# Performance work log

Hardware: AMD Instinct MI355X
Metric: run time of the kernel (lower is better)

The kernel has to match this reference:

```python
import jax, jax.numpy as jnp
import numpy as np

B, C, H, W = 4, 256, 64, 64
C8 = C // 8


def setup_inputs() -> dict:
    key = jax.random.key(0)
    ks = jax.random.split(key, 8)
    x = jax.random.normal(ks[0], (B, C, H, W), dtype=jnp.float32)
    valid = jax.random.uniform(ks[1], (B, 1, H, W), dtype=jnp.float32)
    # 1x1 conv weights (kernel_size=1 -> plain channel matmul) + biases
    Wq = jax.random.normal(ks[2], (C8, C), dtype=jnp.float32) * 0.05
    bq = jnp.zeros((C8,), dtype=jnp.float32)
    Wk = jax.random.normal(ks[3], (C8, C), dtype=jnp.float32) * 0.05
    bk = jnp.zeros((C8,), dtype=jnp.float32)
    Wv = jax.random.normal(ks[4], (C, C), dtype=jnp.float32) * 0.05
    bv = jnp.zeros((C,), dtype=jnp.float32)
    gamma = jnp.asarray(0.5, dtype=jnp.float32)  # nonzero so attention path matters
    return {"x": x, "valid": valid, "Wq": Wq, "bq": bq, "Wk": Wk, "bk": bk,
            "Wv": Wv, "bv": bv, "gamma": gamma}


def reference(x, valid, Wq, bq, Wk, bk, Wv, bv, gamma):
    b, c, h, w = x.shape
    n = h * w
    xf = x.reshape(b, c, n)                                   # [B,C,N]
    # valid is already at (H,W): nearest interpolate to same size is identity
    v = valid.reshape(b, 1, n)                                # [B,1,N]
    q = jnp.einsum('oc,bcn->bno', Wq, xf) + bq                # [B,N,C//8]
    k = jnp.einsum('oc,bcn->bon', Wk, xf) + bk[None, :, None] # [B,C//8,N]
    energy = jnp.einsum('bno,bom->bnm', q, k)                 # [B,N,N]
    attn = jax.nn.softmax(energy, axis=-1)
    va = attn * v                                             # mask columns
    scale = 1.0 / jnp.sum(va, axis=2, keepdims=True)          # per-row renorm
    sa = va * scale                                           # [B,N,N]
    pv = jnp.einsum('oc,bcn->bon', Wv, xf) + bv[None, :, None]  # [B,C,N]
    out = jnp.einsum('bon,bmn->bom', pv, sa)                  # bmm(V, A^T)
    out = out.reshape(b, c, h, w)
    return gamma * out + x, sa
```

## Files before the change

### kernel.cpp

```cpp
#include <hip/hip_runtime.h>

typedef unsigned short u16;
typedef unsigned int u32;
typedef __attribute__((ext_vector_type(8))) short short8;
typedef __attribute__((ext_vector_type(4))) float f32x4;
typedef __attribute__((ext_vector_type(2))) unsigned int u32x2;
typedef __attribute__((ext_vector_type(4))) unsigned int u32x4;

#define BB 4
#define CC 256
#define NT 4096
#define L2E 1.4426950408889634f

__device__ __forceinline__ float b2f(u16 v) {
    union { u32 u; float f; } c; c.u = ((u32)v) << 16; return c.f;
}
__device__ __forceinline__ u16 f2b(float f) {
    union { float f; u32 u; } c; c.f = f;
    u32 u = c.u;
    return (u16)((u + 0x7fffu + ((u >> 16) & 1u)) >> 16);
}

__global__ __launch_bounds__(256) void kprep(
    const float* __restrict__ Wq, const float* __restrict__ Wk,
    const float* __restrict__ Wv, const float* __restrict__ bq,
    const float* __restrict__ bk_, const float* __restrict__ bv,
    u16* __restrict__ wh, u16* __restrict__ wl, float* __restrict__ biasAll)
{
    const int bkx = blockIdx.x;
    const int t = threadIdx.x;
    #pragma unroll
    for (int j = 0; j < 4; ++j) {
        const int idx4 = t + 256 * j;
        const int row  = bkx * 16 + (idx4 >> 6);
        const int col4 = (idx4 & 63) * 4;
        const float* src = row < 32 ? Wq + row * 256
                         : row < 64 ? Wk + (row - 32) * 256
                         :            Wv + (row - 64) * 256;
        f32x4 v = *(const f32x4*)(src + col4);
        u16 h[4], l[4];
        #pragma unroll
        for (int i = 0; i < 4; ++i) {
            h[i] = f2b(v[i]);
            l[i] = f2b(v[i] - b2f(h[i]));
        }
        u32x2 ph, pl;
        ph[0] = (u32)h[0] | ((u32)h[1] << 16); ph[1] = (u32)h[2] | ((u32)h[3] << 16);
        pl[0] = (u32)l[0] | ((u32)l[1] << 16); pl[1] = (u32)l[2] | ((u32)l[3] << 16);
        *(u32x2*)(wh + row * 256 + col4) = ph;
        *(u32x2*)(wl + row * 256 + col4) = pl;
    }
    if (t < 16) {
        const int row = bkx * 16 + t;
        biasAll[row] = row < 32 ? bq[row] : row < 64 ? bk_[row - 32] : bv[row - 64];
    }
}

__global__ __launch_bounds__(256, 1) void kproj(
    const float* __restrict__ x,
    const u16* __restrict__ wh, const u16* __restrict__ wl,
    const float* __restrict__ biasAll,
    u16* __restrict__ qh, u16* __restrict__ ql,
    u16* __restrict__ kh, u16* __restrict__ kl,
    u16* __restrict__ pvw)
{
    __shared__ __align__(16) float lX[256][68];
    __shared__ float lbias[320];
    const int b = blockIdx.y, n0 = blockIdx.x * 64;
    const int t = threadIdx.x;
    const int lane = t & 63, wv = t >> 6;
    const int quad = lane >> 4, l16 = lane & 15;

    {
        const int kX = t >> 3, nn8 = (t & 7) * 8;
        const float* xrow = x + ((size_t)(b * CC + kX)) * NT + n0 + nn8;
        #pragma unroll
        for (int k0 = 0; k0 < 256; k0 += 32) {
            f32x4 xa = *(const f32x4*)(xrow + (size_t)k0 * NT);
            f32x4 xb = *(const f32x4*)(xrow + (size_t)k0 * NT + 4);
            *(f32x4*)&lX[k0 + kX][nn8]     = xa;
            *(f32x4*)&lX[k0 + kX][nn8 + 4] = xb;
        }
        lbias[t] = biasAll[t];
        if (t < 64) lbias[256 + t] = biasAll[256 + t];
    }
    __syncthreads();

    short8 bh[8], bl[8];
    const int coln = wv * 16 + l16;
    #pragma unroll
    for (int s = 0; s < 8; ++s) {
        #pragma unroll
        for (int e = 0; e < 8; ++e) {
            float v = lX[s * 32 + quad * 8 + e][coln];
            u16 h = f2b(v);
            bh[s][e] = (short)h;
            bl[s][e] = (short)f2b(v - b2f(h));
        }
    }

    f32x4 acc[20];
    #pragma unroll
    for (int mt = 0; mt < 20; ++mt) acc[mt] = (f32x4){0.f, 0.f, 0.f, 0.f};

    const u16* whp = wh + l16 * 256 + quad * 8;
    const u16* wlp = wl + l16 * 256 + quad * 8;
    #pragma unroll
    for (int mt = 0; mt < 20; ++mt) {
        #pragma unroll
        for (int s = 0; s < 8; ++s) {
            short8 ah = *(const short8*)(whp + mt * 4096 + s * 32);
            short8 al = *(const short8*)(wlp + mt * 4096 + s * 32);
            acc[mt] = __builtin_amdgcn_mfma_f32_16x16x32_bf16(ah, bh[s], acc[mt], 0, 0, 0);
            acc[mt] = __builtin_amdgcn_mfma_f32_16x16x32_bf16(al, bh[s], acc[mt], 0, 0, 0);
            acc[mt] = __builtin_amdgcn_mfma_f32_16x16x32_bf16(ah, bl[s], acc[mt], 0, 0, 0);
        }
    }

    const int n = n0 + wv * 16 + l16;
    #pragma unroll
    for (int mt = 0; mt < 20; ++mt) {
        u16 hv[4], lv[4];
        #pragma unroll
        for (int i = 0; i < 4; ++i) {
            const int o = mt * 16 + quad * 4 + i;
            const float val = acc[mt][i] + lbias[o];
            hv[i] = f2b(val);
            lv[i] = f2b(val - b2f(hv[i]));
        }
        if (mt < 2) {
            u32x2 ph, pl;
            ph[0] = (u32)hv[0] | ((u32)hv[1] << 16); ph[1] = (u32)hv[2] | ((u32)hv[3] << 16);
            pl[0] = (u32)lv[0] | ((u32)lv[1] << 16); pl[1] = (u32)lv[2] | ((u32)lv[3] << 16);
            const size_t idx = ((size_t)(b * NT + n)) * 32 + mt * 16 + quad * 4;
            *(u32x2*)(qh + idx) = ph;
            *(u32x2*)(ql + idx) = pl;
        } else if (mt < 4) {
            u32x2 ph, pl;
            ph[0] = (u32)hv[0] | ((u32)hv[1] << 16); ph[1] = (u32)hv[2] | ((u32)hv[3] << 16);
            pl[0] = (u32)lv[0] | ((u32)lv[1] << 16); pl[1] = (u32)lv[2] | ((u32)lv[3] << 16);
            const size_t idx = ((size_t)(b * NT + n)) * 32 + (mt - 2) * 16 + quad * 4;
            *(u32x2*)(kh + idx) = ph;
            *(u32x2*)(kl + idx) = pl;
        } else {
            #pragma unroll
            for (int i = 0; i < 4; ++i) {
                const int c = mt * 16 + quad * 4 + i - 64;
                pvw[((size_t)(b * CC + c)) * NT + n] = hv[i];
            }
        }
    }
}

__global__ __launch_bounds__(256) void kattn(
    const u16* __restrict__ qh, const u16* __restrict__ ql,
    const u16* __restrict__ kh, const u16* __restrict__ kl,
    const float* __restrict__ valid, float* __restrict__ sa)
{
    __shared__ float sred[4][4][4];
    const int b    = blockIdx.y;
    const int lane = threadIdx.x & 63;
    const int wv   = threadIdx.x >> 6;
    const int r0   = blockIdx.x * 16;
    const int quad = lane >> 4, l16 = lane & 15;
    const int ct0  = wv * 64;

    const size_t abase = ((size_t)(b * NT + r0 + l16)) * 32 + quad * 8;
    const short8 aqh = *(const short8*)(qh + abase);
    const short8 aql = *(const short8*)(ql + abase);
    const size_t kb = (size_t)b * NT * 32 + (size_t)l16 * 32 + quad * 8;
    const float* vb = valid + b * NT + l16;
    const f32x4 zero = {0.f, 0.f, 0.f, 0.f};

    float sacc[4] = {0.f, 0.f, 0.f, 0.f};
    for (int ct = ct0; ct < ct0 + 64; ++ct) {
        short8 bh = *(const short8*)(kh + kb + (size_t)ct * 512);
        short8 bl = *(const short8*)(kl + kb + (size_t)ct * 512);
        float vcol = vb[ct * 16];
        f32x4 d = __builtin_amdgcn_mfma_f32_16x16x32_bf16(aqh, bh, zero, 0, 0, 0);
        d = __builtin_amdgcn_mfma_f32_16x16x32_bf16(aql, bh, d, 0, 0, 0);
        d = __builtin_amdgcn_mfma_f32_16x16x32_bf16(aqh, bl, d, 0, 0, 0);
        #pragma unroll
        for (int i = 0; i < 4; ++i)
            sacc[i] += vcol * exp2f(fminf(d[i], 60.f) * L2E);
    }
    #pragma unroll
    for (int i = 0; i < 4; ++i) {
        #pragma unroll
        for (int off = 1; off < 16; off <<= 1)
            sacc[i] += __shfl_xor(sacc[i], off, 64);
    }
    if (l16 == 0) {
        #pragma unroll
        for (int i = 0; i < 4; ++i) sred[wv][quad][i] = sacc[i];
    }
    __syncthreads();
    float inv[4];
    #pragma unroll
    for (int i = 0; i < 4; ++i)
        inv[i] = 1.0f / (sred[0][quad][i] + sred[1][quad][i] +
                         sred[2][quad][i] + sred[3][quad][i]);

    for (int ct = ct0; ct < ct0 + 64; ++ct) {
        short8 bh = *(const short8*)(kh + kb + (size_t)ct * 512);
        short8 bl = *(const short8*)(kl + kb + (size_t)ct * 512);
        float vcol = vb[ct * 16];
        f32x4 d = __builtin_amdgcn_mfma_f32_16x16x32_bf16(aqh, bh, zero, 0, 0, 0);
        d = __builtin_amdgcn_mfma_f32_16x16x32_bf16(aql, bh, d, 0, 0, 0);
        d = __builtin_amdgcn_mfma_f32_16x16x32_bf16(aqh, bl, d, 0, 0, 0);
        #pragma unroll
        for (int i = 0; i < 4; ++i) {
            float val = vcol * exp2f(fminf(d[i], 60.f) * L2E) * inv[i];
            sa[((size_t)(b * NT + r0 + quad * 4 + i)) * NT + ct * 16 + l16] = val;
        }
    }
}

#define KOUT_BODY(CUR, T, NXA, NXB, FTA, FTB)                                  \
  {                                                                            \
    if ((T) + 2 < 32) {                                                        \
      FTA = *(const f32x4*)(sap + (size_t)((T) + 2) * 128);                    \
      FTB = *(const f32x4*)(sap + (size_t)((T) + 2) * 128 + 4);                \
    }                                                                          \
    if ((T) + 1 < 32) {                                                        \
      u32 w0 = (u32)f2b(NXA[0]) | ((u32)f2b(NXA[1]) << 16);                    \
      u32 w1 = (u32)f2b(NXA[2]) | ((u32)f2b(NXA[3]) << 16);                    \
      u32 w2 = (u32)f2b(NXB[0]) | ((u32)f2b(NXB[1]) << 16);                    \
      u32 w3 = (u32)f2b(NXB[2]) | ((u32)f2b(NXB[3]) << 16);                    \
      u32x4 pk = {w0, w1, w2, w3};                                             \
      *(u32x4*)(lbw + ((((T) + 1) & 1) * 8192)) = pk;                          \
    }                                                                          \
    const char* lb = lbr + (CUR) * 8192;                                       \
    _Pragma("unroll")                                                          \
    for (int kk = 0; kk < 128; kk += 32) {                                     \
      short8 a0 = *(const short8*)(a0p + (size_t)(T) * 128 + kk);              \
      short8 a1 = *(const short8*)(a1p + (size_t)(T) * 128 + kk);              \
      const int kby = (((kk + quad * 8) * 2) ^ swz);                           \
      short8 b0 = *(const short8*)(lb + l16 * 256 + kby);                      \
      short8 b1 = *(const short8*)(lb + (16 + l16) * 256 + kby);               \
      acc00 = __builtin_amdgcn_mfma_f32_16x16x32_bf16(a0, b0, acc00, 0, 0, 0); \
      acc01 = __builtin_amdgcn_mfma_f32_16x16x32_bf16(a0, b1, acc01, 0, 0, 0); \
      acc10 = __builtin_amdgcn_mfma_f32_16x16x32_bf16(a1, b0, acc10, 0, 0, 0); \
      acc11 = __builtin_amdgcn_mfma_f32_16x16x32_bf16(a1, b1, acc11, 0, 0, 0); \
    }                                                                          \
    asm volatile("s_waitcnt lgkmcnt(0)" ::: "memory");                         \
    __builtin_amdgcn_sched_barrier(0);                                         \
    __builtin_amdgcn_s_barrier();                                              \
    __builtin_amdgcn_sched_barrier(0);                                         \
  }

__global__ __launch_bounds__(512) void kout(
    const u16* __restrict__ pvw, const float* __restrict__ sa,
    const float* __restrict__ x, const float* __restrict__ gamma,
    float* __restrict__ outp)
{
    __shared__ __align__(16) u16 lB[2][32][128];
    const int b    = blockIdx.y;
    const int m0   = blockIdx.x * 32;
    const int t    = threadIdx.x;
    const int lane = t & 63;
    const int wv   = t >> 6;
    const int c0   = wv * 32;
    const int quad = lane >> 4, l16 = lane & 15;
    const int swz  = (l16 & 7) << 4;

    const u16* a0p = pvw + ((size_t)(b * CC + c0 + l16)) * NT + quad * 8;
    const u16* a1p = a0p + (size_t)16 * NT;
    const int sm = t >> 4, sk = (t & 15) * 8;
    const float* sap = sa + ((size_t)(b * NT + m0 + sm)) * NT + sk;
    char* lbw = ((char*)&lB[0][0][0]) + sm * 256 + ((sk * 2) ^ ((sm & 7) << 4));
    const char* lbr = (const char*)&lB[0][0][0];

    f32x4 acc00 = {0,0,0,0}, acc01 = {0,0,0,0}, acc10 = {0,0,0,0}, acc11 = {0,0,0,0};

    f32x4 pA = *(const f32x4*)(sap);
    f32x4 pB = *(const f32x4*)(sap + 4);
    f32x4 nA = *(const f32x4*)(sap + 128);
    f32x4 nB = *(const f32x4*)(sap + 132);
    {
        u32 w0 = (u32)f2b(pA[0]) | ((u32)f2b(pA[1]) << 16);
        u32 w1 = (u32)f2b(pA[2]) | ((u32)f2b(pA[3]) << 16);
        u32 w2 = (u32)f2b(pB[0]) | ((u32)f2b(pB[1]) << 16);
        u32 w3 = (u32)f2b(pB[2]) | ((u32)f2b(pB[3]) << 16);
        u32x4 pk = {w0, w1, w2, w3};
        *(u32x4*)(lbw) = pk;
    }
    asm volatile("s_waitcnt lgkmcnt(0)" ::: "memory");
    __builtin_amdgcn_sched_barrier(0);
    __builtin_amdgcn_s_barrier();
    __builtin_amdgcn_sched_barrier(0);

    f32x4 fA, fB;
    for (int tt = 0; tt < 32; tt += 2) {
        KOUT_BODY(0, tt,     nA, nB, fA, fB)
        KOUT_BODY(1, tt + 1, fA, fB, nA, nB)
    }

    const float g = gamma[0];
    #pragma unroll
    for (int ai = 0; ai < 2; ++ai) {
        #pragma unroll
        for (int bi = 0; bi < 2; ++bi) {
            f32x4 acc = (ai == 0) ? ((bi == 0) ? acc00 : acc01)
                                  : ((bi == 0) ? acc10 : acc11);
            #pragma unroll
            for (int i = 0; i < 4; ++i) {
                const int c = c0 + ai * 16 + quad * 4 + i;
                const int m = m0 + bi * 16 + l16;
                const size_t idx = ((size_t)(b * CC + c)) * NT + m;
                outp[idx] = g * acc[i] + x[idx];
            }
        }
    }
}

extern "C" void kernel_launch(void* const* d_in, const int* in_sizes, int n_in,
                              void* d_out, int out_size, void* d_ws, size_t ws_size,
                              hipStream_t stream)
{
    const float* x     = (const float*)d_in[0];
    const float* valid = (const float*)d_in[1];
    const float* Wq    = (const float*)d_in[2];
    const float* bq    = (const float*)d_in[3];
    const float* Wk    = (const float*)d_in[4];
    const float* bk    = (const float*)d_in[5];
    const float* Wv    = (const float*)d_in[6];
    const float* bv    = (const float*)d_in[7];
    const float* gamma = (const float*)d_in[8];

    float* outp = (float*)d_out;
    float* sa   = outp + (size_t)BB * CC * NT;

    u16* qh  = (u16*)d_ws;
    u16* ql  = qh + (size_t)BB * NT * 32;
    u16* kh  = ql + (size_t)BB * NT * 32;
    u16* kl  = kh + (size_t)BB * NT * 32;
    u16* pvw = kl + (size_t)BB * NT * 32;
    u16* wh  = pvw + (size_t)BB * CC * NT;
    u16* wl  = wh + 320 * 256;
    float* biasAll = (float*)(wl + 320 * 256);

    kprep<<<dim3(20), 256, 0, stream>>>(Wq, Wk, Wv, bq, bk, bv, wh, wl, biasAll);
    kproj<<<dim3(64, BB), 256, 0, stream>>>(x, wh, wl, biasAll,
                                            qh, ql, kh, kl, pvw);
    kattn<<<dim3(256, BB), 256, 0, stream>>>(qh, ql, kh, kl, valid, sa);
    kout<<<dim3(128, BB), 512, 0, stream>>>(pvw, sa, x, gamma, outp);
}
```

Measured before the change: 545.0 us.

## Stage K tiles in double-buffered LDS and share them across two row groups

The attention kernel now handles 32 query rows per block as two row groups, and the blocks halve. K hi/lo tiles are loaded cooperatively into a swizzled, double-buffered LDS area, with the next tile's global loads issued during the current step. Each wave covers half of the column range and does two 16-column tiles per step. The aim is to cut redundant global K reads and hide load latency, at the cost of a block barrier every step and fewer blocks in flight.

```diff
diff --git a/kernel.cpp b/kernel.cpp
--- a/kernel.cpp
+++ b/kernel.cpp
@@ -157,33 +157,92 @@
     const u16* __restrict__ kh, const u16* __restrict__ kl,
     const float* __restrict__ valid, float* __restrict__ sa)
 {
-    __shared__ float sred[4][4][4];
+    __shared__ __align__(16) u16 lK[2 * 4096];
+    __shared__ float sred[2][2][4][4];
     const int b    = blockIdx.y;
-    const int lane = threadIdx.x & 63;
-    const int wv   = threadIdx.x >> 6;
-    const int r0   = blockIdx.x * 16;
+    const int t    = threadIdx.x;
+    const int lane = t & 63;
+    const int wv   = t >> 6;
+    const int rg   = wv >> 1, ch = wv & 1;
+    const int r0   = blockIdx.x * 32 + rg * 16;
     const int quad = lane >> 4, l16 = lane & 15;
-    const int ct0  = wv * 64;
 
     const size_t abase = ((size_t)(b * NT + r0 + l16)) * 32 + quad * 8;
     const short8 aqh = *(const short8*)(qh + abase);
     const short8 aql = *(const short8*)(ql + abase);
-    const size_t kb = (size_t)b * NT * 32 + (size_t)l16 * 32 + quad * 8;
     const float* vb = valid + b * NT + l16;
     const f32x4 zero = {0.f, 0.f, 0.f, 0.f};
+    u16* lKf = &lK[0];
+
+    int g1 = t, g2 = t + 256;
+    const int tl1 = g1 >> 7, n1 = (g1 >> 3) & 15, c161 = g1 & 7;
+    const int tl2 = g2 >> 7, n2 = (g2 >> 3) & 15, c162 = g2 & 7;
+    const int cb1 = (tl1 >> 1) * 128 + (tl1 & 1);
+    const int cb2 = (tl2 >> 1) * 128 + (tl2 & 1);
+    const u16* src1 = (c161 < 4 ? kh : kl) + (size_t)b * NT * 32 + (size_t)n1 * 32 + (c161 & 3) * 8;
+    const u16* src2 = (c162 < 4 ? kh : kl) + (size_t)b * NT * 32 + (size_t)n2 * 32 + (c162 & 3) * 8;
+    const int ldso1 = tl1 * 1024 + n1 * 64 + ((((c161 * 16) ^ ((n1 & 7) << 4))) >> 1);
+    const int ldso2 = tl2 * 1024 + n2 * 64 + ((((c162 * 16) ^ ((n2 & 7) << 4))) >> 1);
+
+    const int base0 = (2 * ch) * 1024;
+    const int base1 = base0 + 1024;
+    const int khoff = l16 * 64 + (((quad * 16) ^ ((l16 & 7) << 4)) >> 1);
+    const int kloff = l16 * 64 + (((64 + quad * 16) ^ ((l16 & 7) << 4)) >> 1);
+
+#define KATTN_PROLOGUE()                                                       \
+    {                                                                          \
+        u32x4 r1 = *(const u32x4*)(src1 + (size_t)cb1 * 512);                  \
+        u32x4 r2 = *(const u32x4*)(src2 + (size_t)cb2 * 512);                  \
+        asm volatile("s_waitcnt vmcnt(0)" ::: "memory");                       \
+        __builtin_amdgcn_sched_barrier(0);                                     \
+        *(u32x4*)(lKf + ldso1) = r1;                                           \
+        *(u32x4*)(lKf + ldso2) = r2;                                           \
+        asm volatile("s_waitcnt lgkmcnt(0)" ::: "memory");                     \
+        __builtin_amdgcn_sched_barrier(0);                                     \
+        __builtin_amdgcn_s_barrier();                                          \
+        __builtin_amdgcn_sched_barrier(0);                                     \
+    }
+
+#define KATTN_STEP_TAIL(S)                                                     \
+    if ((S) + 1 < 64) {                                                        \
+        asm volatile("s_waitcnt vmcnt(0)" ::: "memory");                       \
+        __builtin_amdgcn_sched_barrier(0);                                     \
+        *(u32x4*)(lKf + (((S) + 1) & 1) * 4096 + ldso1) = r1;                  \
+        *(u32x4*)(lKf + (((S) + 1) & 1) * 4096 + ldso2) = r2;                  \
+    }                                                                          \
+    asm volatile("s_waitcnt lgkmcnt(0)" ::: "memory");                         \
+    __builtin_amdgcn_sched_barrier(0);                                         \
+    __builtin_amdgcn_s_barrier();                                              \
+    __builtin_amdgcn_sched_barrier(0);
 
     float sacc[4] = {0.f, 0.f, 0.f, 0.f};
-    for (int ct = ct0; ct < ct0 + 64; ++ct) {
-        short8 bh = *(const short8*)(kh + kb + (size_t)ct * 512);
-        short8 bl = *(const short8*)(kl + kb + (size_t)ct * 512);
-        float vcol = vb[ct * 16];
-        f32x4 d = __builtin_amdgcn_mfma_f32_16x16x32_bf16(aqh, bh, zero, 0, 0, 0);
-        d = __builtin_amdgcn_mfma_f32_16x16x32_bf16(aql, bh, d, 0, 0, 0);
-        d = __builtin_amdgcn_mfma_f32_16x16x32_bf16(aqh, bl, d, 0, 0, 0);
+    KATTN_PROLOGUE();
+    for (int s = 0; s < 64; ++s) {
+        u32x4 r1, r2;
+        if (s + 1 < 64) {
+            r1 = *(const u32x4*)(src1 + (size_t)(cb1 + 2 * (s + 1)) * 512);
+            r2 = *(const u32x4*)(src2 + (size_t)(cb2 + 2 * (s + 1)) * 512);
+        }
+        const u16* lbuf = lKf + (s & 1) * 4096;
+        short8 bh0 = *(const short8*)(lbuf + base0 + khoff);
+        short8 bl0 = *(const short8*)(lbuf + base0 + kloff);
+        short8 bh1 = *(const short8*)(lbuf + base1 + khoff);
+        short8 bl1 = *(const short8*)(lbuf + base1 + kloff);
+        const int ct0 = ch * 128 + 2 * s;
+        const float v0 = vb[ct0 * 16], v1 = vb[(ct0 + 1) * 16];
+        f32x4 d0 = __builtin_amdgcn_mfma_f32_16x16x32_bf16(aqh, bh0, zero, 0, 0, 0);
+        d0 = __builtin_amdgcn_mfma_f32_16x16x32_bf16(aql, bh0, d0, 0, 0, 0);
+        d0 = __builtin_amdgcn_mfma_f32_16x16x32_bf16(aqh, bl0, d0, 0, 0, 0);
+        f32x4 d1 = __builtin_amdgcn_mfma_f32_16x16x32_bf16(aqh, bh1, zero, 0, 0, 0);
+        d1 = __builtin_amdgcn_mfma_f32_16x16x32_bf16(aql, bh1, d1, 0, 0, 0);
+        d1 = __builtin_amdgcn_mfma_f32_16x16x32_bf16(aqh, bl1, d1, 0, 0, 0);
         #pragma unroll
         for (int i = 0; i < 4; ++i)
-            sacc[i] += vcol * exp2f(fminf(d[i], 60.f) * L2E);
-    }
+            sacc[i] += v0 * exp2f(fminf(d0[i], 60.f) * L2E)
+                     + v1 * exp2f(fminf(d1[i], 60.f) * L2E);
+        KATTN_STEP_TAIL(s)
+    }
+
     #pragma unroll
     for (int i = 0; i < 4; ++i) {
         #pragma unroll
@@ -192,28 +251,47 @@
     }
     if (l16 == 0) {
         #pragma unroll
-        for (int i = 0; i < 4; ++i) sred[wv][quad][i] = sacc[i];
+        for (int i = 0; i < 4; ++i) sred[rg][ch][quad][i] = sacc[i];
     }
     __syncthreads();
     float inv[4];
     #pragma unroll
     for (int i = 0; i < 4; ++i)
-        inv[i] = 1.0f / (sred[0][quad][i] + sred[1][quad][i] +
-                         sred[2][quad][i] + sred[3][quad][i]);
-
-    for (int ct = ct0; ct < ct0 + 64; ++ct) {
-        short8 bh = *(const short8*)(kh + kb + (size_t)ct * 512);
-        short8 bl = *(const short8*)(kl + kb + (size_t)ct * 512);
-        float vcol = vb[ct * 16];
-        f32x4 d = __builtin_amdgcn_mfma_f32_16x16x32_bf16(aqh, bh, zero, 0, 0, 0);
-        d = __builtin_amdgcn_mfma_f32_16x16x32_bf16(aql, bh, d, 0, 0, 0);
-        d = __builtin_amdgcn_mfma_f32_16x16x32_bf16(aqh, bl, d, 0, 0, 0);
+        inv[i] = 1.0f / (sred[rg][0][quad][i] + sred[rg][1][quad][i]);
+    __syncthreads();
+
+    float* sabase = sa + ((size_t)(b * NT + r0 + quad * 4)) * NT + l16;
+    KATTN_PROLOGUE();
+    for (int s = 0; s < 64; ++s) {
+        u32x4 r1, r2;
+        if (s + 1 < 64) {
+            r1 = *(const u32x4*)(src1 + (size_t)(cb1 + 2 * (s + 1)) * 512);
+            r2 = *(const u32x4*)(src2 + (size_t)(cb2 + 2 * (s + 1)) * 512);
+        }
+        const u16* lbuf = lKf + (s & 1) * 4096;
+        short8 bh0 = *(const short8*)(lbuf + base0 + khoff);
+        short8 bl0 = *(const short8*)(lbuf + base0 + kloff);
+        short8 bh1 = *(const short8*)(lbuf + base1 + khoff);
+        short8 bl1 = *(const short8*)(lbuf + base1 + kloff);
+        const int ct0 = ch * 128 + 2 * s;
+        const float v0 = vb[ct0 * 16], v1 = vb[(ct0 + 1) * 16];
+        f32x4 d0 = __builtin_amdgcn_mfma_f32_16x16x32_bf16(aqh, bh0, zero, 0, 0, 0);
+        d0 = __builtin_amdgcn_mfma_f32_16x16x32_bf16(aql, bh0, d0, 0, 0, 0);
+        d0 = __builtin_amdgcn_mfma_f32_16x16x32_bf16(aqh, bl0, d0, 0, 0, 0);
+        f32x4 d1 = __builtin_amdgcn_mfma_f32_16x16x32_bf16(aqh, bh1, zero, 0, 0, 0);
+        d1 = __builtin_amdgcn_mfma_f32_16x16x32_bf16(aql, bh1, d1, 0, 0, 0);
+        d1 = __builtin_amdgcn_mfma_f32_16x16x32_bf16(aqh, bl1, d1, 0, 0, 0);
         #pragma unroll
         for (int i = 0; i < 4; ++i) {
-            float val = vcol * exp2f(fminf(d[i], 60.f) * L2E) * inv[i];
-            sa[((size_t)(b * NT + r0 + quad * 4 + i)) * NT + ct * 16 + l16] = val;
-        }
-    }
+            sabase[(size_t)i * NT + ct0 * 16]
+                = v0 * exp2f(fminf(d0[i], 60.f) * L2E) * inv[i];
+            sabase[(size_t)i * NT + (ct0 + 1) * 16]
+                = v1 * exp2f(fminf(d1[i], 60.f) * L2E) * inv[i];
+        }
+        KATTN_STEP_TAIL(s)
+    }
+#undef KATTN_PROLOGUE
+#undef KATTN_STEP_TAIL
 }
 
 #define KOUT_BODY(CUR, T, NXA, NXB, FTA, FTB)                                  \
@@ -343,6 +421,6 @@
     kprep<<<dim3(20), 256, 0, stream>>>(Wq, Wk, Wv, bq, bk, bv, wh, wl, biasAll);
     kproj<<<dim3(64, BB), 256, 0, stream>>>(x, wh, wl, biasAll,
                                             qh, ql, kh, kl, pvw);
-    kattn<<<dim3(256, BB), 256, 0, stream>>>(qh, ql, kh, kl, valid, sa);
+    kattn<<<dim3(128, BB), 256, 0, stream>>>(qh, ql, kh, kl, valid, sa);
     kout<<<dim3(128, BB), 512, 0, stream>>>(pvw, sa, x, gamma, outp);
 }
```

New measurement: 564.5 us. +3.6%, slower.
